# Optimization experiments

Measured on AMD Instinct MI355X. Metric: run time of the kernel, lower is better.

The kernel has to match this reference:

```python
import jax, jax.numpy as jnp
import numpy as np

B, T, D, H, O = 1024, 2048, 13, 128, 2


def setup_inputs() -> dict:
    key = jax.random.key(0)
    k1, k2, k3, k4 = jax.random.split(key, 4)
    xs = jax.random.normal(k1, (B, T, D), dtype=jnp.float32)
    # nn.Linear(in, out, bias=False) weights: [out, in]
    W_in = jax.random.normal(k2, (H, D), dtype=jnp.float32) / np.sqrt(D).astype(np.float32)
    W_h = jax.random.normal(k3, (H, H), dtype=jnp.float32) / np.sqrt(H).astype(np.float32)
    W_out = jax.random.normal(k4, (O, H), dtype=jnp.float32) / np.sqrt(H).astype(np.float32)
    return {"xs": xs, "W_in": W_in, "W_h": W_h, "W_out": W_out}


def reference(xs, W_in, W_h, W_out):
    # Vanilla hardtanh RNN, h0 = 0 (first step y = hardtanh(in_h(x)) == hardtanh(in_h(x) + W_h @ 0)).
    # Precompute all input projections in one big GEMM: [B, T, H]
    pre = jnp.einsum('btd,hd->bth', xs, W_in)

    def step(h, xh_t):  # h: [B, H], xh_t: [B, H]
        h = jnp.clip(xh_t + h @ W_h.T, -1.0, 1.0)  # F.hardtanh
        return h, None

    h0 = jnp.zeros((xs.shape[0], W_in.shape[0]), dtype=xs.dtype)
    hT, _ = jax.lax.scan(step, h0, jnp.swapaxes(pre, 0, 1))  # scan over time
    # Only the final hidden state per sequence is projected to the output.
    return hT @ W_out.T  # [B, O]
```

## Files before the change

### kernel.cpp

```cpp
#include <hip/hip_runtime.h>
#include <stdint.h>


#define RNN_B 1024
#define RNN_T 2048
#define RNN_D 13
#define RNN_H 128
#define RNN_O 2

#define NB 16
#define NWAVE 4
#define NTHR (NWAVE * 64)
#define ROWS 136

using f32x4 = __attribute__((ext_vector_type(4))) float;
using v8s   = __attribute__((ext_vector_type(8))) short;

__device__ __forceinline__ short f2bf(float f) {
    union { float f; uint32_t u; } c; c.f = f;
    uint32_t u = c.u + 0x7fffu + ((c.u >> 16) & 1u);
    return (short)(u >> 16);
}
__device__ __forceinline__ float bf2fs(short s) {
    union { uint32_t u; float f; } c; c.u = ((uint32_t)(uint16_t)s) << 16;
    return c.f;
}
__device__ __forceinline__ float bitf(uint32_t u) {
    union { uint32_t u; float f; } c; c.u = u; return c.f;
}
__device__ __forceinline__ uint32_t cvtpk(float a, float b) {
    uint32_t r;
    asm("v_cvt_pk_bf16_f32 %0, %1, %2" : "=v"(r) : "v"(a), "v"(b));
    return r;
}
__device__ __forceinline__ v8s pack4(uint32_t a, uint32_t b, uint32_t c, uint32_t d) {
    union { uint32_t u[4]; v8s s; } z;
    z.u[0] = a; z.u[1] = b; z.u[2] = c; z.u[3] = d; return z.s;
}
__device__ __forceinline__ float clamp1(float v) {
    return __builtin_amdgcn_fmed3f(v, -1.0f, 1.0f);
}

#define STEP(CUR, NXT, X0, X1, X2, X3, TPF)                                      \
  do {                                                                           \
    v8s bh[4], bl[4];                                                            \
    bh[0] = *(const v8s*)&Hhi[CUR][n][g8];                                       \
    bh[1] = *(const v8s*)&Hhi[CUR][n][32 + g8];                                  \
    bh[2] = *(const v8s*)&Hhi[CUR][n][64 + g8];                                  \
    bh[3] = *(const v8s*)&Hhi[CUR][n][96 + g8];                                  \
    bl[0] = *(const v8s*)&Hlo[CUR][n][g8];                                       \
    bl[1] = *(const v8s*)&Hlo[CUR][n][32 + g8];                                  \
    bl[2] = *(const v8s*)&Hlo[CUR][n][64 + g8];                                  \
    bl[3] = *(const v8s*)&Hlo[CUR][n][96 + g8];                                  \
    float m0 = X0, m1 = X1, m2 = X2, m3 = X3;                                    \
    if (g == 3) { m1 = 0.0f; m2 = 0.0f; m3 = 0.0f; }                             \
    uint32_t xh01 = cvtpk(m0, m1), xh23 = cvtpk(m2, m3);                         \
    float q0 = m0 - bitf(xh01 << 16);                                            \
    float q1 = m1 - bitf(xh01 & 0xffff0000u);                                    \
    float q2 = m2 - bitf(xh23 << 16);                                            \
    float q3 = m3 - bitf(xh23 & 0xffff0000u);                                    \
    uint32_t xl01 = cvtpk(q0, q1), xl23 = cvtpk(q2, q3);                         \
    v8s xh = pack4(xh01, xh23, 0u, 0u);                                          \
    v8s xl = pack4(xl01, xl23, 0u, 0u);                                          \
    if ((TPF) < RNN_T) {                                                         \
      const float* xp = xrow + (size_t)(TPF) * RNN_D;                            \
      X0 = xp[d0]; X1 = xp[d1]; X2 = xp[d2]; X3 = xp[d3];                        \
    }                                                                            \
    f32x4 A1 = {0.f,0.f,0.f,0.f};                                                \
    f32x4 A2 = A1, A3 = A1, B1 = A1, B2 = A1, B3 = A1;                           \
    _Pragma("unroll")                                                            \
    for (int kt = 0; kt < 4; ++kt) {                                             \
      A1 = __builtin_amdgcn_mfma_f32_16x16x32_bf16(whiA[kt], bh[kt], A1, 0,0,0); \
      B1 = __builtin_amdgcn_mfma_f32_16x16x32_bf16(whiB[kt], bh[kt], B1, 0,0,0); \
      A2 = __builtin_amdgcn_mfma_f32_16x16x32_bf16(whiA[kt], bl[kt], A2, 0,0,0); \
      B2 = __builtin_amdgcn_mfma_f32_16x16x32_bf16(whiB[kt], bl[kt], B2, 0,0,0); \
      A3 = __builtin_amdgcn_mfma_f32_16x16x32_bf16(wloA[kt], bh[kt], A3, 0,0,0); \
      B3 = __builtin_amdgcn_mfma_f32_16x16x32_bf16(wloB[kt], bh[kt], B3, 0,0,0); \
    }                                                                            \
    A1 = __builtin_amdgcn_mfma_f32_16x16x32_bf16(whiA[4], xh, A1, 0,0,0);        \
    B1 = __builtin_amdgcn_mfma_f32_16x16x32_bf16(whiB[4], xh, B1, 0,0,0);        \
    A2 = __builtin_amdgcn_mfma_f32_16x16x32_bf16(whiA[4], xl, A2, 0,0,0);        \
    B2 = __builtin_amdgcn_mfma_f32_16x16x32_bf16(whiB[4], xl, B2, 0,0,0);        \
    A3 = __builtin_amdgcn_mfma_f32_16x16x32_bf16(wloA[4], xh, A3, 0,0,0);        \
    B3 = __builtin_amdgcn_mfma_f32_16x16x32_bf16(wloB[4], xh, B3, 0,0,0);        \
    {                                                                            \
      float v0 = clamp1(A1[0] + A2[0] + A3[0]);                                  \
      float v1 = clamp1(A1[1] + A2[1] + A3[1]);                                  \
      float v2 = clamp1(A1[2] + A2[2] + A3[2]);                                  \
      float v3 = clamp1(A1[3] + A2[3] + A3[3]);                                  \
      uint32_t h01 = cvtpk(v0, v1), h23 = cvtpk(v2, v3);                         \
      float p0 = v0 - bitf(h01 << 16);                                           \
      float p1 = v1 - bitf(h01 & 0xffff0000u);                                   \
      float p2 = v2 - bitf(h23 << 16);                                           \
      float p3 = v3 - bitf(h23 & 0xffff0000u);                                   \
      uint32_t l01 = cvtpk(p0, p1), l23 = cvtpk(p2, p3);                         \
      int2 wv; wv.x = (int)h01; wv.y = (int)h23;                                 \
      *(int2*)&Hhi[NXT][n][wbase + g8] = wv;                                     \
      wv.x = (int)l01; wv.y = (int)l23;                                          \
      *(int2*)&Hlo[NXT][n][wbase + g8] = wv;                                     \
    }                                                                            \
    {                                                                            \
      float v0 = clamp1(B1[0] + B2[0] + B3[0]);                                  \
      float v1 = clamp1(B1[1] + B2[1] + B3[1]);                                  \
      float v2 = clamp1(B1[2] + B2[2] + B3[2]);                                  \
      float v3 = clamp1(B1[3] + B2[3] + B3[3]);                                  \
      uint32_t h01 = cvtpk(v0, v1), h23 = cvtpk(v2, v3);                         \
      float p0 = v0 - bitf(h01 << 16);                                           \
      float p1 = v1 - bitf(h01 & 0xffff0000u);                                   \
      float p2 = v2 - bitf(h23 << 16);                                           \
      float p3 = v3 - bitf(h23 & 0xffff0000u);                                   \
      uint32_t l01 = cvtpk(p0, p1), l23 = cvtpk(p2, p3);                         \
      int2 wv; wv.x = (int)h01; wv.y = (int)h23;                                 \
      *(int2*)&Hhi[NXT][n][wbase + g8 + 4] = wv;                                 \
      wv.x = (int)l01; wv.y = (int)l23;                                          \
      *(int2*)&Hlo[NXT][n][wbase + g8 + 4] = wv;                                 \
    }                                                                            \
    __syncthreads();                                                             \
  } while (0)

__global__ __launch_bounds__(NTHR, 1) void rnn_mfma6_kernel(
    const float* __restrict__ xs,
    const float* __restrict__ W_in,
    const float* __restrict__ W_h,
    const float* __restrict__ W_out,
    float* __restrict__ out)
{
    __shared__ __align__(16) short Hhi[2][NB][ROWS];
    __shared__ __align__(16) short Hlo[2][NB][ROWS];

    const int tid  = threadIdx.x;
    const int lane = tid & 63;
    const int wid  = tid >> 6;
    const int n    = lane & 15;
    const int g    = lane >> 4;
    const int g8   = g * 8;
    const int wbase = 32 * wid;
    const int b0   = blockIdx.x * NB;

    const int d0 = (4 * g + 0 > 12) ? 12 : 4 * g + 0;
    const int d1 = (4 * g + 1 > 12) ? 12 : 4 * g + 1;
    const int d2 = (4 * g + 2 > 12) ? 12 : 4 * g + 2;
    const int d3 = (4 * g + 3 > 12) ? 12 : 4 * g + 3;

    v8s whiA[5], wloA[5], whiB[5], wloB[5];
    #pragma unroll
    for (int mi = 0; mi < 2; ++mi) {
        const int row = 16 * (wid * 2 + mi) + n;
        #pragma unroll
        for (int kt = 0; kt < 5; ++kt) {
            v8s h8, l8;
            #pragma unroll
            for (int j = 0; j < 4; ++j) {
                float w1, w2;
                if (kt < 4) {
                    w1 = W_h[row * RNN_H + 32 * kt + 4 * g + j];
                    w2 = W_h[row * RNN_H + 32 * kt + 16 + 4 * g + j];
                } else {
                    const int kx = 4 * g + j;
                    w1 = (kx < RNN_D) ? W_in[row * RNN_D + kx] : 0.0f;
                    w2 = 0.0f;
                }
                const short h1 = f2bf(w1);
                const short h2 = f2bf(w2);
                h8[j] = h1; h8[4 + j] = h2;
                l8[j] = f2bf(w1 - bf2fs(h1));
                l8[4 + j] = f2bf(w2 - bf2fs(h2));
            }
            if (mi == 0) { whiA[kt] = h8; wloA[kt] = l8; }
            else         { whiB[kt] = h8; wloB[kt] = l8; }
        }
    }

    for (int idx = tid; idx < NB * ROWS; idx += NTHR) {
        (&Hhi[0][0][0])[idx] = 0;
        (&Hlo[0][0][0])[idx] = 0;
    }

    const float* xrow = xs + (size_t)(b0 + n) * RNN_T * RNN_D;
    float xa0 = xrow[d0], xa1 = xrow[d1], xa2 = xrow[d2], xa3 = xrow[d3];
    float xb0 = xrow[RNN_D + d0], xb1 = xrow[RNN_D + d1];
    float xb2 = xrow[RNN_D + d2], xb3 = xrow[RNN_D + d3];
    __syncthreads();

    for (int t = 0; t < RNN_T; t += 2) {
        STEP(0, 1, xa0, xa1, xa2, xa3, t + 2);
        STEP(1, 0, xb0, xb1, xb2, xb3, t + 3);
    }

    if (wid == 0 && lane < NB * RNN_O) {
        const int nn = lane & 15;
        const int o  = lane >> 4;
        float acc = 0.0f;
        for (int i = 0; i < RNN_H; ++i) {
            const int pos = 32 * (i >> 5) + 8 * ((i >> 2) & 3)
                          + 4 * ((i >> 4) & 1) + (i & 3);
            const float hv = bf2fs(Hhi[0][nn][pos]) + bf2fs(Hlo[0][nn][pos]);
            acc = fmaf(W_out[o * RNN_H + i], hv, acc);
        }
        out[(size_t)(b0 + nn) * RNN_O + o] = acc;
    }
}

extern "C" void kernel_launch(void* const* d_in, const int* in_sizes, int n_in,
                              void* d_out, int out_size, void* d_ws, size_t ws_size,
                              hipStream_t stream) {
    const float* xs    = (const float*)d_in[0];
    const float* W_in  = (const float*)d_in[1];
    const float* W_h   = (const float*)d_in[2];
    const float* W_out = (const float*)d_in[3];
    float* out = (float*)d_out;

    rnn_mfma6_kernel<<<RNN_B / NB, NTHR, 0, stream>>>(xs, W_in, W_h, W_out, out);
}
```

Baseline: 1.242 ms.

## Split hidden rows across eight waves, one 16-row tile per wave

Doubles the waves per block from four to eight, so each wave computes one 16-row output tile instead of two. This halves the serial MFMA chain and the epilogue work per wave on each recurrent step. The cost is twice as many waves taking part in the per-step barrier and redundant per-wave LDS reads of the shared hidden state. The __syncthreads is replaced with an explicit lgkmcnt wait plus s_barrier, fenced by sched barriers, and launch bounds change to allow two blocks per CU.

```diff
diff --git a/kernel.cpp b/kernel.cpp
--- a/kernel.cpp
+++ b/kernel.cpp
@@ -9,7 +9,7 @@
 #define RNN_O 2
 
 #define NB 16
-#define NWAVE 4
+#define NWAVE 8
 #define NTHR (NWAVE * 64)
 #define ROWS 136
 
@@ -39,6 +39,14 @@
 }
 __device__ __forceinline__ float clamp1(float v) {
     return __builtin_amdgcn_fmed3f(v, -1.0f, 1.0f);
+}
+
+__device__ __forceinline__ void barrier_lgkm() {
+    __builtin_amdgcn_sched_barrier(0);
+    asm volatile("s_waitcnt lgkmcnt(0)" ::: "memory");
+    __builtin_amdgcn_s_barrier();
+    asm volatile("" ::: "memory");
+    __builtin_amdgcn_sched_barrier(0);
 }
 
 #define STEP(CUR, NXT, X0, X1, X2, X3, TPF)                                      \
@@ -67,22 +75,16 @@
       X0 = xp[d0]; X1 = xp[d1]; X2 = xp[d2]; X3 = xp[d3];                        \
     }                                                                            \
     f32x4 A1 = {0.f,0.f,0.f,0.f};                                                \
-    f32x4 A2 = A1, A3 = A1, B1 = A1, B2 = A1, B3 = A1;                           \
+    f32x4 A2 = A1, A3 = A1;                                                      \
     _Pragma("unroll")                                                            \
     for (int kt = 0; kt < 4; ++kt) {                                             \
-      A1 = __builtin_amdgcn_mfma_f32_16x16x32_bf16(whiA[kt], bh[kt], A1, 0,0,0); \
-      B1 = __builtin_amdgcn_mfma_f32_16x16x32_bf16(whiB[kt], bh[kt], B1, 0,0,0); \
-      A2 = __builtin_amdgcn_mfma_f32_16x16x32_bf16(whiA[kt], bl[kt], A2, 0,0,0); \
-      B2 = __builtin_amdgcn_mfma_f32_16x16x32_bf16(whiB[kt], bl[kt], B2, 0,0,0); \
-      A3 = __builtin_amdgcn_mfma_f32_16x16x32_bf16(wloA[kt], bh[kt], A3, 0,0,0); \
-      B3 = __builtin_amdgcn_mfma_f32_16x16x32_bf16(wloB[kt], bh[kt], B3, 0,0,0); \
+      A1 = __builtin_amdgcn_mfma_f32_16x16x32_bf16(whi[kt], bh[kt], A1, 0,0,0);  \
+      A2 = __builtin_amdgcn_mfma_f32_16x16x32_bf16(whi[kt], bl[kt], A2, 0,0,0);  \
+      A3 = __builtin_amdgcn_mfma_f32_16x16x32_bf16(wlo[kt], bh[kt], A3, 0,0,0);  \
     }                                                                            \
-    A1 = __builtin_amdgcn_mfma_f32_16x16x32_bf16(whiA[4], xh, A1, 0,0,0);        \
-    B1 = __builtin_amdgcn_mfma_f32_16x16x32_bf16(whiB[4], xh, B1, 0,0,0);        \
-    A2 = __builtin_amdgcn_mfma_f32_16x16x32_bf16(whiA[4], xl, A2, 0,0,0);        \
-    B2 = __builtin_amdgcn_mfma_f32_16x16x32_bf16(whiB[4], xl, B2, 0,0,0);        \
-    A3 = __builtin_amdgcn_mfma_f32_16x16x32_bf16(wloA[4], xh, A3, 0,0,0);        \
-    B3 = __builtin_amdgcn_mfma_f32_16x16x32_bf16(wloB[4], xh, B3, 0,0,0);        \
+    A1 = __builtin_amdgcn_mfma_f32_16x16x32_bf16(whi[4], xh, A1, 0,0,0);         \
+    A2 = __builtin_amdgcn_mfma_f32_16x16x32_bf16(whi[4], xl, A2, 0,0,0);         \
+    A3 = __builtin_amdgcn_mfma_f32_16x16x32_bf16(wlo[4], xh, A3, 0,0,0);         \
     {                                                                            \
       float v0 = clamp1(A1[0] + A2[0] + A3[0]);                                  \
       float v1 = clamp1(A1[1] + A2[1] + A3[1]);                                  \
@@ -95,30 +97,14 @@
       float p3 = v3 - bitf(h23 & 0xffff0000u);                                   \
       uint32_t l01 = cvtpk(p0, p1), l23 = cvtpk(p2, p3);                         \
       int2 wv; wv.x = (int)h01; wv.y = (int)h23;                                 \
-      *(int2*)&Hhi[NXT][n][wbase + g8] = wv;                                     \
+      *(int2*)&Hhi[NXT][n][wp] = wv;                                             \
       wv.x = (int)l01; wv.y = (int)l23;                                          \
-      *(int2*)&Hlo[NXT][n][wbase + g8] = wv;                                     \
+      *(int2*)&Hlo[NXT][n][wp] = wv;                                             \
     }                                                                            \
-    {                                                                            \
-      float v0 = clamp1(B1[0] + B2[0] + B3[0]);                                  \
-      float v1 = clamp1(B1[1] + B2[1] + B3[1]);                                  \
-      float v2 = clamp1(B1[2] + B2[2] + B3[2]);                                  \
-      float v3 = clamp1(B1[3] + B2[3] + B3[3]);                                  \
-      uint32_t h01 = cvtpk(v0, v1), h23 = cvtpk(v2, v3);                         \
-      float p0 = v0 - bitf(h01 << 16);                                           \
-      float p1 = v1 - bitf(h01 & 0xffff0000u);                                   \
-      float p2 = v2 - bitf(h23 << 16);                                           \
-      float p3 = v3 - bitf(h23 & 0xffff0000u);                                   \
-      uint32_t l01 = cvtpk(p0, p1), l23 = cvtpk(p2, p3);                         \
-      int2 wv; wv.x = (int)h01; wv.y = (int)h23;                                 \
-      *(int2*)&Hhi[NXT][n][wbase + g8 + 4] = wv;                                 \
-      wv.x = (int)l01; wv.y = (int)l23;                                          \
-      *(int2*)&Hlo[NXT][n][wbase + g8 + 4] = wv;                                 \
-    }                                                                            \
-    __syncthreads();                                                             \
+    barrier_lgkm();                                                              \
   } while (0)
 
-__global__ __launch_bounds__(NTHR, 1) void rnn_mfma6_kernel(
+__global__ __launch_bounds__(NTHR, 2) void rnn_mfma7_kernel(
     const float* __restrict__ xs,
     const float* __restrict__ W_in,
     const float* __restrict__ W_h,
@@ -134,7 +120,7 @@
     const int n    = lane & 15;
     const int g    = lane >> 4;
     const int g8   = g * 8;
-    const int wbase = 32 * wid;
+    const int wp   = 32 * (wid >> 1) + g8 + 4 * (wid & 1);
     const int b0   = blockIdx.x * NB;
 
     const int d0 = (4 * g + 0 > 12) ? 12 : 4 * g + 0;
@@ -142,10 +128,9 @@
     const int d2 = (4 * g + 2 > 12) ? 12 : 4 * g + 2;
     const int d3 = (4 * g + 3 > 12) ? 12 : 4 * g + 3;
 
-    v8s whiA[5], wloA[5], whiB[5], wloB[5];
-    #pragma unroll
-    for (int mi = 0; mi < 2; ++mi) {
-        const int row = 16 * (wid * 2 + mi) + n;
+    v8s whi[5], wlo[5];
+    {
+        const int row = 16 * wid + n;
         #pragma unroll
         for (int kt = 0; kt < 5; ++kt) {
             v8s h8, l8;
@@ -166,8 +151,8 @@
                 l8[j] = f2bf(w1 - bf2fs(h1));
                 l8[4 + j] = f2bf(w2 - bf2fs(h2));
             }
-            if (mi == 0) { whiA[kt] = h8; wloA[kt] = l8; }
-            else         { whiB[kt] = h8; wloB[kt] = l8; }
+            whi[kt] = h8;
+            wlo[kt] = l8;
         }
     }
 
@@ -186,6 +171,8 @@
         STEP(0, 1, xa0, xa1, xa2, xa3, t + 2);
         STEP(1, 0, xb0, xb1, xb2, xb3, t + 3);
     }
+
+    __syncthreads();
 
     if (wid == 0 && lane < NB * RNN_O) {
         const int nn = lane & 15;
@@ -210,5 +197,5 @@
     const float* W_out = (const float*)d_in[3];
     float* out = (float*)d_out;
 
-    rnn_mfma6_kernel<<<RNN_B / NB, NTHR, 0, stream>>>(xs, W_in, W_h, W_out, out);
-}
+    rnn_mfma7_kernel<<<RNN_B / NB, NTHR, 0, stream>>>(xs, W_in, W_h, W_out, out);
+}
```

Measured after the change: 1.784 ms. +43.7%, slower.
